# Kernel tuning notes

Hardware: AMD Instinct MI355X
Metric: run time of the kernel (lower is better)

## Reference

```python
import jax, jax.numpy as jnp
import numpy as np

LAMBDA_IDENTITY = 1.0
LAMBDA_ATTENTION = 0.5

B, F_FRAMES, N, V = 4, 16, 1024, 4


def setup_inputs() -> dict:
    key = jax.random.key(0)
    k1, k2, k3, k4, k5, k6 = jax.random.split(key, 6)
    refined_points = jax.random.normal(k1, (B, F_FRAMES, N, 3), dtype=jnp.float32)
    gt_points = jax.random.normal(k2, (B, F_FRAMES, N, 3), dtype=jnp.float32)
    visibility = jax.random.randint(k3, (B, F_FRAMES, N), 0, 2, dtype=jnp.int32)
    projection_matrices = jax.random.normal(k4, (V, B, 3, 4), dtype=jnp.float32)
    tracks_2d = jax.random.normal(k5, (V, B, F_FRAMES, N, 2), dtype=jnp.float32)
    correspondence_matrices = jax.random.normal(k6, (V, V, B, N, N), dtype=jnp.float32)
    return {
        'refined_points': refined_points,
        'gt_points': gt_points,
        'visibility': visibility,
        'projection_matrices': projection_matrices,
        'tracks_2d': tracks_2d,
        'correspondence_matrices': correspondence_matrices,
    }


def _reconstruction_loss(pred, gt, visibility):
    mask = (visibility > 0)[..., None]                       # [B,F,N,1]
    se = (pred - gt) ** 2                                    # [B,F,N,3]
    num = jnp.sum(mask) * 3                                  # number of masked scalar elements
    big = jnp.float32(1e30)
    mn = jnp.min(jnp.where(mask, gt, big), axis=(0, 1, 2))   # per-coord min over valid points
    mx = jnp.max(jnp.where(mask, gt, -big), axis=(0, 1, 2))
    scale = jnp.max(mx - mn) + 1e-6
    scale = jnp.where(num > 0, scale, jnp.float32(1.0))
    scale = jax.lax.stop_gradient(scale)
    mse_mean = jnp.sum(jnp.where(mask, se, 0.0)) / jnp.maximum(num, 1)
    return mse_mean / scale ** 2


def _identity_loss(pred, proj, tracks):
    # pred [B,F,N,3], proj [V,B,3,4], tracks [V,B,F,N,2]
    ones = jnp.ones(pred.shape[:-1] + (1,), dtype=pred.dtype)
    homo = jnp.concatenate([pred, ones], axis=-1)            # [B,F,N,4]
    p2h = jnp.einsum('vbij,bfnj->vbfni', proj, homo)         # [V,B,F,N,3]
    p2 = p2h[..., :2] / (p2h[..., 2:3] + 1e-10)              # [V,B,F,N,2]
    valid = jnp.sum(jnp.abs(tracks), axis=-1) > 1e-6         # [V,B,F,N]
    vmask = valid[..., None]
    big = jnp.float32(1e30)
    mn = jnp.min(jnp.where(vmask, tracks, big), axis=3)      # [V,B,F,2]
    mx = jnp.max(jnp.where(vmask, tracks, -big), axis=3)
    wh = jnp.maximum(224.0, mx - mn + 1e-6)                  # (width, height)
    any_valid = jnp.any(valid, axis=3)[..., None]
    wh = jnp.where(any_valid, wh, 224.0)
    wh = jax.lax.stop_gradient(wh)
    err = ((p2 - tracks) / wh[:, :, :, None, :]) ** 2        # [V,B,F,N,2]
    view_loss = jnp.mean(jnp.sum(err, axis=-1), axis=-1)     # [V,B,F]
    return jnp.mean(view_loss)


def _attention_loss(corr, visibility):
    # corr [V,V,B,N,N] logits; visibility [B,F,N]
    n = corr.shape[-1]
    vis = visibility[:, 0, :n] > 0                           # frame 0 visibility [B,N]
    idx = jnp.arange(n)
    d = jnp.abs(idx[:, None] - idx[None, :])
    band = jnp.where(d == 0, 1.0,
           jnp.where(d == 1, 0.7,
           jnp.where(d == 2, 0.49, 0.0))).astype(jnp.float32)   # [N,N]
    pair = jnp.logical_or(vis[:, :, None], vis[:, None, :])     # [B,N,N]
    gt_corr = band[None] * pair.astype(jnp.float32)             # [B,N,N]
    weights = 1.0 + 2.0 * gt_corr
    x = corr
    # stable BCE-with-logits, elementwise weight, mean reduction per matrix
    bce = weights * (jnp.maximum(x, 0.0) - x * gt_corr + jnp.log1p(jnp.exp(-jnp.abs(x))))
    per = jnp.mean(bce, axis=(-1, -2))                          # [V,V,B]
    return jnp.mean(per)                                        # sum / count with count = V*V*B


def reference(refined_points, gt_points, visibility, projection_matrices, tracks_2d, correspondence_matrices):
    rec = _reconstruction_loss(refined_points, gt_points, visibility)
    ident = _identity_loss(refined_points, projection_matrices, tracks_2d)
    att = _attention_loss(correspondence_matrices, visibility)
    total = 1.0 * rec + LAMBDA_IDENTITY * ident + LAMBDA_ATTENTION * att
    return total, rec, ident, att
```

## Files before the change

kernel.cpp:

```cpp
#include <hip/hip_runtime.h>
#include <math.h>

#define B_ 4
#define F_ 16
#define N_ 1024
#define V_ 4

#define ATT_BLOCKS 4096
#define REC_BLOCKS 256
#define ID_BLOCKS  256

typedef float vf4 __attribute__((ext_vector_type(4)));


__device__ __forceinline__ float softplusf(float x) {
    float ax = fabsf(x);
    float e = __expf(-ax);
    return fmaxf(x, 0.0f) + __logf(1.0f + e);
}

__global__ __launch_bounds__(256) void mega_kernel(const float* __restrict__ pred,
                                                   const float* __restrict__ gt,
                                                   const int* __restrict__ vis,
                                                   const float* __restrict__ proj,
                                                   const float* __restrict__ tracks,
                                                   const float* __restrict__ corr,
                                                   double* __restrict__ attp,
                                                   float* __restrict__ recp,
                                                   float* __restrict__ idp) {
    const int blk = blockIdx.x;
    const int t = threadIdx.x;
    const int wave = t >> 6, lane = t & 63;

    if (blk < ATT_BLOCKS) {
        const int b = (blk >> 6) & 3;
        const int row0 = (blk & 63) << 4;

        const vf4* base4 = (const vf4*)corr + (size_t)blk * 4096;
        vf4 d[16];
        #pragma unroll
        for (int k = 0; k < 16; k++)
            d[k] = __builtin_nontemporal_load(base4 + k * 256 + t);

        __shared__ unsigned char vs[N_];
        {
            int4 v4 = ((const int4*)(vis + b * (F_ * N_)))[t];
            vs[4 * t + 0] = v4.x > 0;
            vs[4 * t + 1] = v4.y > 0;
            vs[4 * t + 2] = v4.z > 0;
            vs[4 * t + 3] = v4.w > 0;
        }

        vf4 sx = {0.f, 0.f, 0.f, 0.f};
        vf4 st = {0.f, 0.f, 0.f, 0.f};
        vf4 pr = {1.f, 1.f, 1.f, 1.f};
        #pragma unroll
        for (int k = 0; k < 16; k++) {
            vf4 x = d[k];
            vf4 tt;
            tt.x = fabsf(x.x); tt.y = fabsf(x.y); tt.z = fabsf(x.z); tt.w = fabsf(x.w);
            vf4 e;
            e.x = __expf(-tt.x); e.y = __expf(-tt.y); e.z = __expf(-tt.z); e.w = __expf(-tt.w);
            sx += x;
            st += tt;
            pr = pr + pr * e;
        }
        float acc = 0.5f * ((sx.x + sx.y + sx.z + sx.w) + (st.x + st.y + st.z + st.w))
                  + (__logf(pr.x) + __logf(pr.y)) + (__logf(pr.z) + __logf(pr.w));

        __syncthreads();

        const int j0 = 4 * t;
        if (j0 >= row0 - 5 && j0 <= row0 + 17) {
            #pragma unroll
            for (int k = 0; k < 16; k++) {
                const int i = row0 + k;
                if (j0 < i - 5 || j0 > i + 2) continue;
                unsigned char vi = vs[i];
                float xs[4] = {d[k].x, d[k].y, d[k].z, d[k].w};
                #pragma unroll
                for (int kk = 0; kk < 4; kk++) {
                    int j = j0 + kk;
                    int dd = (i > j) ? (i - j) : (j - i);
                    if (dd <= 2) {
                        if (vi | vs[j]) {
                            float g = (dd == 0) ? 1.0f : ((dd == 1) ? 0.7f : 0.49f);
                            float sp = softplusf(xs[kk]);
                            acc += 2.f * g * sp - (1.f + 2.f * g) * xs[kk] * g;
                        }
                    }
                }
            }
        }

        #pragma unroll
        for (int off = 32; off; off >>= 1) acc += __shfl_down(acc, off);
        __shared__ double sw[4];
        if (lane == 0) sw[wave] = (double)acc;
        __syncthreads();
        if (t == 0) attp[blk] = (sw[0] + sw[1]) + (sw[2] + sw[3]);

    } else if (blk < ATT_BLOCKS + REC_BLOCKS) {
        const int r = blk - ATT_BLOCKS;
        const int p = r * 256 + t;
        bool m = vis[p] > 0;
        float gx = gt[3 * p], gy = gt[3 * p + 1], gz = gt[3 * p + 2];
        float px = pred[3 * p], py = pred[3 * p + 1], pz = pred[3 * p + 2];
        float se = 0.f;
        if (m) {
            float dx = px - gx, dy = py - gy, dz = pz - gz;
            se = dx * dx + dy * dy + dz * dz;
        }
        float mn0 = m ? gx : 1e30f, mn1 = m ? gy : 1e30f, mn2 = m ? gz : 1e30f;
        float mx0 = m ? gx : -1e30f, mx1 = m ? gy : -1e30f, mx2 = m ? gz : -1e30f;
        float c = m ? 1.f : 0.f;
        #pragma unroll
        for (int off = 32; off; off >>= 1) {
            se += __shfl_down(se, off);
            c  += __shfl_down(c, off);
            mn0 = fminf(mn0, __shfl_down(mn0, off));
            mn1 = fminf(mn1, __shfl_down(mn1, off));
            mn2 = fminf(mn2, __shfl_down(mn2, off));
            mx0 = fmaxf(mx0, __shfl_down(mx0, off));
            mx1 = fmaxf(mx1, __shfl_down(mx1, off));
            mx2 = fmaxf(mx2, __shfl_down(mx2, off));
        }
        __shared__ float sh[4][8];
        if (lane == 0) {
            sh[wave][0] = se; sh[wave][1] = c;
            sh[wave][2] = mn0; sh[wave][3] = mn1; sh[wave][4] = mn2;
            sh[wave][5] = mx0; sh[wave][6] = mx1; sh[wave][7] = mx2;
        }
        __syncthreads();
        if (t == 0) {
            se = sh[0][0]; c = sh[0][1];
            mn0 = sh[0][2]; mn1 = sh[0][3]; mn2 = sh[0][4];
            mx0 = sh[0][5]; mx1 = sh[0][6]; mx2 = sh[0][7];
            for (int w = 1; w < 4; w++) {
                se += sh[w][0]; c += sh[w][1];
                mn0 = fminf(mn0, sh[w][2]); mn1 = fminf(mn1, sh[w][3]); mn2 = fminf(mn2, sh[w][4]);
                mx0 = fmaxf(mx0, sh[w][5]); mx1 = fmaxf(mx1, sh[w][6]); mx2 = fmaxf(mx2, sh[w][7]);
            }
            float* o = recp + r * 8;
            o[0] = se; o[1] = c;
            o[2] = mn0; o[3] = mn1; o[4] = mn2;
            o[5] = mx0; o[6] = mx1; o[7] = mx2;
        }

    } else {
        const int idx = blk - (ATT_BLOCKS + REC_BLOCKS);
        const int v = idx / (B_ * F_);
        const int b = (idx / F_) % B_;
        const int f = idx % F_;
        const float* P = proj + ((size_t)(v * B_ + b)) * 12;
        const float* T = tracks + ((size_t)((v * B_ + b) * F_ + f)) * N_ * 2;
        const float* Q = pred + ((size_t)(b * F_ + f)) * N_ * 3;

        float mnx = 1e30f, mny = 1e30f, mxx = -1e30f, mxy = -1e30f;
        for (int n = t; n < N_; n += 256) {
            float tx = T[2 * n], ty = T[2 * n + 1];
            if ((fabsf(tx) + fabsf(ty)) > 1e-6f) {
                mnx = fminf(mnx, tx); mxx = fmaxf(mxx, tx);
                mny = fminf(mny, ty); mxy = fmaxf(mxy, ty);
            }
        }
        #pragma unroll
        for (int off = 32; off; off >>= 1) {
            mnx = fminf(mnx, __shfl_down(mnx, off));
            mxx = fmaxf(mxx, __shfl_down(mxx, off));
            mny = fminf(mny, __shfl_down(mny, off));
            mxy = fmaxf(mxy, __shfl_down(mxy, off));
        }
        __shared__ float shi[4][4];
        __shared__ float wh[2];
        if (lane == 0) { shi[wave][0] = mnx; shi[wave][1] = mxx; shi[wave][2] = mny; shi[wave][3] = mxy; }
        __syncthreads();
        if (t == 0) {
            float a = shi[0][0], bb = shi[0][1], c = shi[0][2], d = shi[0][3];
            for (int w = 1; w < 4; w++) {
                a = fminf(a, shi[w][0]); bb = fmaxf(bb, shi[w][1]);
                c = fminf(c, shi[w][2]); d = fmaxf(d, shi[w][3]);
            }
            wh[0] = fmaxf(224.0f, bb - a + 1e-6f);
            wh[1] = fmaxf(224.0f, d - c + 1e-6f);
        }
        __syncthreads();
        float whx = wh[0], why = wh[1];

        float P00 = P[0], P01 = P[1], P02 = P[2], P03 = P[3];
        float P10 = P[4], P11 = P[5], P12 = P[6], P13 = P[7];
        float P20 = P[8], P21 = P[9], P22 = P[10], P23 = P[11];

        float errsum = 0.f;
        for (int n = t; n < N_; n += 256) {
            float x = Q[3 * n], y = Q[3 * n + 1], z = Q[3 * n + 2];
            float p0 = P00 * x + P01 * y + P02 * z + P03;
            float p1 = P10 * x + P11 * y + P12 * z + P13;
            float p2 = P20 * x + P21 * y + P22 * z + P23;
            float den = p2 + 1e-10f;
            float tx = T[2 * n], ty = T[2 * n + 1];
            float ex = (p0 / den - tx) / whx;
            float ey = (p1 / den - ty) / why;
            errsum += ex * ex + ey * ey;
        }
        #pragma unroll
        for (int off = 32; off; off >>= 1) errsum += __shfl_down(errsum, off);
        __shared__ float se2[4];
        if (lane == 0) se2[wave] = errsum;
        __syncthreads();
        if (t == 0) idp[idx] = (se2[0] + se2[1] + se2[2] + se2[3]) / (float)N_;
    }
}

__global__ __launch_bounds__(256) void fin_kernel(const double* __restrict__ attp,
                                                  const float* __restrict__ recp,
                                                  const float* __restrict__ idp,
                                                  float* __restrict__ out) {
    const int t = threadIdx.x;
    const int wave = t >> 6, lane = t & 63;

    double a = 0.0;
    #pragma unroll
    for (int k = 0; k < ATT_BLOCKS / 256; k++) a += attp[k * 256 + t];
    const float* rp = recp + t * 8;
    double se = (double)rp[0];
    double c  = (double)rp[1];
    float mn0 = rp[2], mn1 = rp[3], mn2 = rp[4];
    float mx0 = rp[5], mx1 = rp[6], mx2 = rp[7];
    double id = (double)idp[t];

    #pragma unroll
    for (int off = 32; off; off >>= 1) {
        a  += __shfl_down(a, off);
        se += __shfl_down(se, off);
        c  += __shfl_down(c, off);
        id += __shfl_down(id, off);
        mn0 = fminf(mn0, __shfl_down(mn0, off));
        mn1 = fminf(mn1, __shfl_down(mn1, off));
        mn2 = fminf(mn2, __shfl_down(mn2, off));
        mx0 = fmaxf(mx0, __shfl_down(mx0, off));
        mx1 = fmaxf(mx1, __shfl_down(mx1, off));
        mx2 = fmaxf(mx2, __shfl_down(mx2, off));
    }
    __shared__ double sa[4], sse[4], sc[4], sid[4];
    __shared__ float smn[3][4], smx[3][4];
    if (lane == 0) {
        sa[wave] = a; sse[wave] = se; sc[wave] = c; sid[wave] = id;
        smn[0][wave] = mn0; smn[1][wave] = mn1; smn[2][wave] = mn2;
        smx[0][wave] = mx0; smx[1][wave] = mx1; smx[2][wave] = mx2;
    }
    __syncthreads();
    if (t == 0) {
        a = sa[0]; se = sse[0]; c = sc[0]; id = sid[0];
        mn0 = smn[0][0]; mn1 = smn[1][0]; mn2 = smn[2][0];
        mx0 = smx[0][0]; mx1 = smx[1][0]; mx2 = smx[2][0];
        for (int w = 1; w < 4; w++) {
            a += sa[w]; se += sse[w]; c += sc[w]; id += sid[w];
            mn0 = fminf(mn0, smn[0][w]); mn1 = fminf(mn1, smn[1][w]); mn2 = fminf(mn2, smn[2][w]);
            mx0 = fmaxf(mx0, smx[0][w]); mx1 = fmaxf(mx1, smx[1][w]); mx2 = fmaxf(mx2, smx[2][w]);
        }
        double num = c * 3.0;
        double mse = se / fmax(num, 1.0);
        float rng = fmaxf(mx0 - mn0, fmaxf(mx1 - mn1, mx2 - mn2));
        float scale = rng + 1e-6f;
        if (c < 0.5) scale = 1.0f;
        float rec = (float)mse / (scale * scale);
        float ident = (float)(id / (double)(V_ * B_ * F_));
        float att = (float)(a / ((double)V_ * V_ * B_ * N_ * N_));
        float total = rec + 1.0f * ident + 0.5f * att;
        out[0] = total; out[1] = rec; out[2] = ident; out[3] = att;
    }
}

extern "C" void kernel_launch(void* const* d_in, const int* in_sizes, int n_in,
                              void* d_out, int out_size, void* d_ws, size_t ws_size,
                              hipStream_t stream) {
    const float* refined = (const float*)d_in[0];
    const float* gtp     = (const float*)d_in[1];
    const int*   vis     = (const int*)d_in[2];
    const float* proj    = (const float*)d_in[3];
    const float* tracks  = (const float*)d_in[4];
    const float* corr    = (const float*)d_in[5];
    float* out = (float*)d_out;

    double* attp = (double*)d_ws;
    float*  recp = (float*)((char*)d_ws + 32768);
    float*  idp  = (float*)((char*)d_ws + 40960);

    mega_kernel<<<ATT_BLOCKS + REC_BLOCKS + ID_BLOCKS, 256, 0, stream>>>(
        refined, gtp, vis, proj, tracks, corr, attp, recp, idp);
    fin_kernel<<<1, 256, 0, stream>>>(attp, recp, idp, out);
}
```

Baseline: 378.2 us.

## Process 64 rows per attention block with double-buffered register prefetch

Attention blocks now cover 64 rows of a correspondence matrix instead of 16, which cuts the block count from 4096 to 1024. Each block loads 8 rows at a time into two register buffers and prefetches the next chunk while computing the current one. This is meant to overlap memory latency with the exp/log math and to amortize per-block setup and the final reduction. The cost is higher register pressure and fewer blocks in flight, which may lower occupancy; the workspace offsets are shrunk to match the smaller partial array.

```diff
diff --git a/kernel.cpp b/kernel.cpp
--- a/kernel.cpp
+++ b/kernel.cpp
@@ -6,7 +6,7 @@
 #define N_ 1024
 #define V_ 4
 
-#define ATT_BLOCKS 4096
+#define ATT_BLOCKS 1024
 #define REC_BLOCKS 256
 #define ID_BLOCKS  256
 
@@ -33,14 +33,17 @@
     const int wave = t >> 6, lane = t & 63;
 
     if (blk < ATT_BLOCKS) {
-        const int b = (blk >> 6) & 3;
-        const int row0 = (blk & 63) << 4;
-
-        const vf4* base4 = (const vf4*)corr + (size_t)blk * 4096;
-        vf4 d[16];
-        #pragma unroll
-        for (int k = 0; k < 16; k++)
-            d[k] = __builtin_nontemporal_load(base4 + k * 256 + t);
+        const int m = blk >> 4;
+        const int g = blk & 15;
+        const int b = m & 3;
+        const int rbase = g << 6;
+
+        const vf4* mat4 = (const vf4*)corr + (size_t)m * (N_ * N_ / 4);
+
+        vf4 A[8], Bb[8];
+        #pragma unroll
+        for (int rr = 0; rr < 8; rr++)
+            A[rr] = __builtin_nontemporal_load(mat4 + (rbase + rr) * 256 + t);
 
         __shared__ unsigned char vs[N_];
         {
@@ -50,49 +53,61 @@
             vs[4 * t + 2] = v4.z > 0;
             vs[4 * t + 3] = v4.w > 0;
         }
-
+        __syncthreads();
+
+        const int j0 = 4 * t;
         vf4 sx = {0.f, 0.f, 0.f, 0.f};
         vf4 st = {0.f, 0.f, 0.f, 0.f};
         vf4 pr = {1.f, 1.f, 1.f, 1.f};
-        #pragma unroll
-        for (int k = 0; k < 16; k++) {
-            vf4 x = d[k];
-            vf4 tt;
-            tt.x = fabsf(x.x); tt.y = fabsf(x.y); tt.z = fabsf(x.z); tt.w = fabsf(x.w);
-            vf4 e;
-            e.x = __expf(-tt.x); e.y = __expf(-tt.y); e.z = __expf(-tt.z); e.w = __expf(-tt.w);
-            sx += x;
-            st += tt;
-            pr = pr + pr * e;
-        }
-        float acc = 0.5f * ((sx.x + sx.y + sx.z + sx.w) + (st.x + st.y + st.z + st.w))
-                  + (__logf(pr.x) + __logf(pr.y)) + (__logf(pr.z) + __logf(pr.w));
-
-        __syncthreads();
-
-        const int j0 = 4 * t;
-        if (j0 >= row0 - 5 && j0 <= row0 + 17) {
+        float acc = 0.f;
+
+        #pragma unroll
+        for (int c = 0; c < 8; c++) {
+            vf4* cur = (c & 1) ? Bb : A;
+            vf4* nxt = (c & 1) ? A : Bb;
+            const int r0 = rbase + c * 8;
+            if (c < 7) {
+                #pragma unroll
+                for (int rr = 0; rr < 8; rr++)
+                    nxt[rr] = __builtin_nontemporal_load(mat4 + (r0 + 8 + rr) * 256 + t);
+            }
             #pragma unroll
-            for (int k = 0; k < 16; k++) {
-                const int i = row0 + k;
-                if (j0 < i - 5 || j0 > i + 2) continue;
-                unsigned char vi = vs[i];
-                float xs[4] = {d[k].x, d[k].y, d[k].z, d[k].w};
+            for (int rr = 0; rr < 8; rr++) {
+                vf4 x = cur[rr];
+                vf4 tt;
+                tt.x = fabsf(x.x); tt.y = fabsf(x.y); tt.z = fabsf(x.z); tt.w = fabsf(x.w);
+                vf4 e;
+                e.x = __expf(-tt.x); e.y = __expf(-tt.y); e.z = __expf(-tt.z); e.w = __expf(-tt.w);
+                sx += x;
+                st += tt;
+                pr = pr + pr * e;
+            }
+            if (j0 >= r0 - 5 && j0 <= r0 + 9) {
                 #pragma unroll
-                for (int kk = 0; kk < 4; kk++) {
-                    int j = j0 + kk;
-                    int dd = (i > j) ? (i - j) : (j - i);
-                    if (dd <= 2) {
-                        if (vi | vs[j]) {
-                            float g = (dd == 0) ? 1.0f : ((dd == 1) ? 0.7f : 0.49f);
-                            float sp = softplusf(xs[kk]);
-                            acc += 2.f * g * sp - (1.f + 2.f * g) * xs[kk] * g;
+                for (int rr = 0; rr < 8; rr++) {
+                    const int i = r0 + rr;
+                    if (j0 < i - 5 || j0 > i + 2) continue;
+                    unsigned char vi = vs[i];
+                    float xs[4] = {cur[rr].x, cur[rr].y, cur[rr].z, cur[rr].w};
+                    #pragma unroll
+                    for (int kk = 0; kk < 4; kk++) {
+                        int j = j0 + kk;
+                        int dd = (i > j) ? (i - j) : (j - i);
+                        if (dd <= 2) {
+                            if (vi | vs[j]) {
+                                float gq = (dd == 0) ? 1.0f : ((dd == 1) ? 0.7f : 0.49f);
+                                float sp = softplusf(xs[kk]);
+                                acc += 2.f * gq * sp - (1.f + 2.f * gq) * xs[kk] * gq;
+                            }
                         }
                     }
                 }
             }
         }
 
+        acc += 0.5f * ((sx.x + sx.y + sx.z + sx.w) + (st.x + st.y + st.z + st.w))
+             + (__logf(pr.x) + __logf(pr.y)) + (__logf(pr.z) + __logf(pr.w));
+
         #pragma unroll
         for (int off = 32; off; off >>= 1) acc += __shfl_down(acc, off);
         __shared__ double sw[4];
@@ -103,17 +118,17 @@
     } else if (blk < ATT_BLOCKS + REC_BLOCKS) {
         const int r = blk - ATT_BLOCKS;
         const int p = r * 256 + t;
-        bool m = vis[p] > 0;
+        bool mk = vis[p] > 0;
         float gx = gt[3 * p], gy = gt[3 * p + 1], gz = gt[3 * p + 2];
         float px = pred[3 * p], py = pred[3 * p + 1], pz = pred[3 * p + 2];
         float se = 0.f;
-        if (m) {
+        if (mk) {
             float dx = px - gx, dy = py - gy, dz = pz - gz;
             se = dx * dx + dy * dy + dz * dz;
         }
-        float mn0 = m ? gx : 1e30f, mn1 = m ? gy : 1e30f, mn2 = m ? gz : 1e30f;
-        float mx0 = m ? gx : -1e30f, mx1 = m ? gy : -1e30f, mx2 = m ? gz : -1e30f;
-        float c = m ? 1.f : 0.f;
+        float mn0 = mk ? gx : 1e30f, mn1 = mk ? gy : 1e30f, mn2 = mk ? gz : 1e30f;
+        float mx0 = mk ? gx : -1e30f, mx1 = mk ? gy : -1e30f, mx2 = mk ? gz : -1e30f;
+        float c = mk ? 1.f : 0.f;
         #pragma unroll
         for (int off = 32; off; off >>= 1) {
             se += __shfl_down(se, off);
@@ -284,8 +299,8 @@
     float* out = (float*)d_out;
 
     double* attp = (double*)d_ws;
-    float*  recp = (float*)((char*)d_ws + 32768);
-    float*  idp  = (float*)((char*)d_ws + 40960);
+    float*  recp = (float*)((char*)d_ws + 8192);
+    float*  idp  = (float*)((char*)d_ws + 16384);
 
     mega_kernel<<<ATT_BLOCKS + REC_BLOCKS + ID_BLOCKS, 256, 0, stream>>>(
         refined, gtp, vis, proj, tracks, corr, attp, recp, idp);
```

Measured after the change: 910.8 us. +140.8%, slower.
